# Optimization experiments

Hardware: AMD Instinct MI355X
Metric: run time of the kernel (lower is better)

## Reference

```python
import jax, jax.numpy as jnp
import numpy as np


def setup_inputs() -> dict:
    key = jax.random.key(0)
    k1, k2, k3 = jax.random.split(key, 3)
    B, C, H, W = 16, 256, 32, 32
    K, D = 8192, 256
    z = jax.random.normal(k1, (B, C, H, W), dtype=jnp.float32)
    # torch init: uniform(-1/K, 1/K); use small-scale values for realism
    embedding = jax.random.uniform(k2, (K, D), dtype=jnp.float32,
                                   minval=-1.0 / K, maxval=1.0 / K)
    proj_w = jax.random.normal(k3, (D, D), dtype=jnp.float32) * (1.0 / np.sqrt(D))
    return {"z": z, "embedding": embedding, "proj_w": proj_w}


def reference(z, embedding, proj_w):
    commitment_cost = 0.25
    B, C, H, W = z.shape
    # codebook = Linear(embedding) with no bias: emb @ W^T  -> [K, D]
    codebook = embedding @ proj_w.T
    zt = jnp.transpose(z, (0, 2, 3, 1))            # [B, H, W, C]
    zf = zt.reshape(-1, C)                          # [N, C], N = B*H*W
    # squared distances: ||z||^2 + ||e||^2 - 2 z.e  -> [N, K]
    d = (jnp.sum(zf * zf, axis=1, keepdims=True)
         + jnp.sum(codebook * codebook, axis=1)
         - 2.0 * jnp.einsum('nd,kd->nk', zf, codebook))
    min_encoding_indices = jnp.argmin(d, axis=1)    # [N]
    z_quantized = codebook[min_encoding_indices].reshape(zt.shape)  # [B,H,W,C]
    commitment_loss = commitment_cost * jnp.mean(
        (jax.lax.stop_gradient(z_quantized) - zt) ** 2)
    codebook_loss = jnp.mean((z_quantized - jax.lax.stop_gradient(zt)) ** 2)
    loss = commitment_loss + codebook_loss
    # straight-through estimator
    zq_st = zt + jax.lax.stop_gradient(z_quantized - zt)
    out = jnp.transpose(zq_st, (0, 3, 1, 2))        # [B, C, H, W]
    idx = min_encoding_indices.reshape(B, H, W)
    return out, loss, commitment_loss, codebook_loss, idx
```

## Files before the change

### kernel.cpp

```cpp
#include <hip/hip_runtime.h>
#include <cfloat>


constexpr int Dd = 256;
constexpr float INV_M = 1.0f / 4194304.0f;
constexpr float DLT = 1e-3f;

typedef unsigned short u16;
typedef unsigned int u32;
typedef __attribute__((ext_vector_type(8))) short short8;
typedef __attribute__((ext_vector_type(4))) float f32x4;

#define GLOBAL_AS __attribute__((address_space(1)))
#define LDS_AS    __attribute__((address_space(3)))

__device__ __forceinline__ unsigned monof(float f) {
  unsigned u = __float_as_uint(f);
  return (u & 0x80000000u) ? ~u : (u | 0x80000000u);
}
__device__ __forceinline__ float unmonof(unsigned p) {
  unsigned u = (p & 0x80000000u) ? (p & 0x7FFFFFFFu) : ~p;
  return __uint_as_float(u);
}
__device__ __forceinline__ u16 f2bf(float x) {
  unsigned u = __float_as_uint(x);
  u += 0x7FFFu + ((u >> 16) & 1u);
  return (u16)(u >> 16);
}

__global__ __launch_bounds__(256)
void k_codebook(const float* __restrict__ emb, const float* __restrict__ proj,
                float* __restrict__ cb, u16* __restrict__ eh) {
  __shared__ float et[64 * 65];
  __shared__ float pt[64 * 65];
  const int t = threadIdx.x;
  const int tx = t & 15, ty = t >> 4;
  const int kb = blockIdx.x * 64;
  const int db = blockIdx.y * 64;
  float acc[4][4];
#pragma unroll
  for (int u = 0; u < 4; ++u)
#pragma unroll
    for (int v = 0; v < 4; ++v) acc[u][v] = 0.f;

  const int jm = t & 15;
  const int q  = t >> 4;

  for (int jc = 0; jc < Dd; jc += 64) {
    __syncthreads();
#pragma unroll
    for (int i = 0; i < 4; ++i) {
      const int row = q + i * 16;
      const float4 e4 = *(const float4*)(emb  + (size_t)(kb + row) * Dd + jc + jm * 4);
      const float4 p4 = *(const float4*)(proj + (size_t)(db + row) * Dd + jc + jm * 4);
      et[(jm*4 + 0) * 65 + row] = e4.x;
      et[(jm*4 + 1) * 65 + row] = e4.y;
      et[(jm*4 + 2) * 65 + row] = e4.z;
      et[(jm*4 + 3) * 65 + row] = e4.w;
      pt[(jm*4 + 0) * 65 + row] = p4.x;
      pt[(jm*4 + 1) * 65 + row] = p4.y;
      pt[(jm*4 + 2) * 65 + row] = p4.z;
      pt[(jm*4 + 3) * 65 + row] = p4.w;
    }
    __syncthreads();
#pragma unroll 16
    for (int j = 0; j < 64; ++j) {
      float a[4], b[4];
#pragma unroll
      for (int u = 0; u < 4; ++u) a[u] = et[j*65 + ty*4 + u];
#pragma unroll
      for (int v = 0; v < 4; ++v) b[v] = pt[j*65 + tx*4 + v];
#pragma unroll
      for (int u = 0; u < 4; ++u)
#pragma unroll
        for (int v = 0; v < 4; ++v) acc[u][v] = fmaf(a[u], b[v], acc[u][v]);
    }
  }
#pragma unroll
  for (int u = 0; u < 4; ++u) {
    const int k = kb + ty*4 + u;
#pragma unroll
    for (int v = 0; v < 4; ++v) {
      const int d = db + tx*4 + v;
      const float val = acc[u][v];
      cb[(size_t)k * Dd + d] = val;
      eh[(size_t)k * Dd + d] = f2bf(val);
    }
  }
}

__global__ __launch_bounds__(256)
void k_norms(const float* __restrict__ cb, float* __restrict__ norms) {
  const int k = blockIdx.x * 256 + threadIdx.x;
  const float* row = cb + (size_t)k * Dd;
  float s = 0.f;
  for (int d = 0; d < Dd; d += 4) {
    const float4 v = *(const float4*)(row + d);
    s = fmaf(v.x, v.x, s);
    s = fmaf(v.y, v.y, s);
    s = fmaf(v.z, v.z, s);
    s = fmaf(v.w, v.w, s);
  }
  norms[k] = s;
}

__global__ __launch_bounds__(256)
void k_prep_z(const float* __restrict__ z, u16* __restrict__ zh,
              float* __restrict__ znorm) {
  __shared__ float tile[256 * 33];
  const int t = threadIdx.x;
  const int blk = blockIdx.x;
  const int w = t & 31, rg = t >> 5;
  const size_t zbase = (size_t)(blk >> 5) * 262144 + (size_t)(blk & 31) * 32 + w;
#pragma unroll 8
  for (int i = 0; i < 32; ++i) {
    const int d = rg * 32 + i;
    tile[d * 33 + w] = z[zbase + (size_t)d * 1024];
  }
  __syncthreads();
  if (t < 32) {
    float s = 0.f;
    for (int d = 0; d < Dd; ++d) {
      const float v = tile[d * 33 + t];
      s = fmaf(v, v, s);
    }
    znorm[blk * 32 + t] = s;
  }
  const int nl = t >> 3, seg = t & 7;
  const size_t obase = (size_t)(blk * 32 + nl) * Dd + seg * 32;
#pragma unroll
  for (int j = 0; j < 4; ++j) {
    u16 hb[8];
#pragma unroll
    for (int e = 0; e < 8; ++e)
      hb[e] = f2bf(tile[(seg * 32 + j * 8 + e) * 33 + nl]);
    *(uint4*)(zh + obase + j * 8) = *(const uint4*)hb;
  }
}

template <bool EMIT>
__global__ __launch_bounds__(256, 2)
void k_scan(const u16* __restrict__ zh, const u16* __restrict__ eh,
            const float* __restrict__ norms, const float* __restrict__ znorm,
            u32* __restrict__ rowminG, const float* __restrict__ rowThr,
            u32* __restrict__ rowcnt, u16* __restrict__ slots) {
  __shared__ u16 zs[64 * 256];
  __shared__ u16 es[256 * 64];
  const int t    = threadIdx.x;
  const int lane = t & 63;
  const int ml   = lane & 15;
  const int qd   = lane >> 4;
  const int wvu  = __builtin_amdgcn_readfirstlane(t >> 6);
  const int rowhalf = wvu & 1;
  const int colhalf = wvu >> 1;
  const int bid  = blockIdx.x;
  const int kb   = (bid & 7) * 1024;
  const int nb   = (bid >> 3) * 64;

#pragma unroll
  for (int i = 0; i < 8; ++i) {
    const int r0 = wvu * 16 + i * 2;
    const int row_l = r0 + (lane >> 5);
    const int c = (lane & 31) ^ ((row_l & 7) << 2);
    const u16* gp = zh + (size_t)(nb + row_l) * 256 + c * 8;
    __builtin_amdgcn_global_load_lds((const GLOBAL_AS void*)gp,
                                     (LDS_AS void*)(zs + r0 * 256), 16, 0, 0);
  }

  float zn[2][4], thr[2][4];
#pragma unroll
  for (int rt = 0; rt < 2; ++rt) {
    const int nr = nb + rowhalf * 32 + rt * 16 + qd * 4;
    const f32x4 z4 = *(const f32x4*)(znorm + nr);
#pragma unroll
    for (int r = 0; r < 4; ++r) zn[rt][r] = z4[r];
    if (EMIT) {
      const f32x4 t4 = *(const f32x4*)(rowThr + nr);
#pragma unroll
      for (int r = 0; r < 4; ++r) thr[rt][r] = t4[r];
    }
  }

  float mv[2][4];
#pragma unroll
  for (int rt = 0; rt < 2; ++rt)
#pragma unroll
    for (int r = 0; r < 4; ++r) mv[rt][r] = FLT_MAX;

#pragma unroll 1
  for (int kt = 0; kt < 4; ++kt) {
    f32x4 acc[2][8];
#pragma unroll
    for (int rt = 0; rt < 2; ++rt)
#pragma unroll
      for (int ct = 0; ct < 8; ++ct) acc[rt][ct] = (f32x4)0.f;

#pragma unroll 1
    for (int dh = 0; dh < 4; ++dh) {
      __syncthreads();
#pragma unroll
      for (int i = 0; i < 8; ++i) {
        const int colbase = wvu * 64 + i * 8;
        const int col_l = colbase + (lane >> 3);
        const int c = (lane & 7) ^ (col_l & 7);
        const u16* gp = eh + (size_t)(kb + kt * 256 + col_l) * 256 + dh * 64 + c * 8;
        __builtin_amdgcn_global_load_lds((const GLOBAL_AS void*)gp,
                                         (LDS_AS void*)(es + colbase * 64), 16, 0, 0);
      }
      __syncthreads();

#pragma unroll
      for (int dc2 = 0; dc2 < 2; ++dc2) {
        short8 Af[2], Bf[8];
#pragma unroll
        for (int rt = 0; rt < 2; ++rt) {
          const int row_l = rowhalf * 32 + rt * 16 + ml;
          const int cg = dh * 8 + dc2 * 4 + qd;
          const int slot = cg ^ ((row_l & 7) << 2);
          Af[rt] = *(const short8*)(zs + row_l * 256 + slot * 8);
        }
#pragma unroll
        for (int ct = 0; ct < 8; ++ct) {
          const int col_l = colhalf * 128 + ct * 16 + ml;
          const int c = dc2 * 4 + qd;
          const int slot = c ^ (col_l & 7);
          Bf[ct] = *(const short8*)(es + col_l * 64 + slot * 8);
        }
#pragma unroll
        for (int rt = 0; rt < 2; ++rt)
#pragma unroll
          for (int ct = 0; ct < 8; ++ct)
            acc[rt][ct] = __builtin_amdgcn_mfma_f32_16x16x32_bf16(
                Af[rt], Bf[ct], acc[rt][ct], 0, 0, 0);
      }
    }

#pragma unroll
    for (int ct = 0; ct < 8; ++ct) {
      const int k = kb + kt * 256 + colhalf * 128 + ct * 16 + ml;
      const float nk = norms[k];
#pragma unroll
      for (int rt = 0; rt < 2; ++rt)
#pragma unroll
        for (int r = 0; r < 4; ++r) {
          const float sc = (zn[rt][r] + nk) - 2.0f * acc[rt][ct][r];
          if (!EMIT) {
            mv[rt][r] = fminf(mv[rt][r], sc);
          } else if (sc <= thr[rt][r]) {
            const int n = nb + rowhalf * 32 + rt * 16 + qd * 4 + r;
            const u32 pos = atomicAdd(&rowcnt[n], 1u);
            if (pos < 32u) slots[n * 32 + pos] = (u16)k;
          }
        }
    }
  }

  if (!EMIT) {
#pragma unroll
    for (int rt = 0; rt < 2; ++rt)
#pragma unroll
      for (int r = 0; r < 4; ++r) {
        float m = mv[rt][r];
#pragma unroll
        for (int s = 1; s < 16; s <<= 1) m = fminf(m, __shfl_xor(m, s, 64));
        if (ml == 0)
          atomicMin(&rowminG[nb + rowhalf * 32 + rt * 16 + qd * 4 + r], monof(m));
      }
  }
}

__global__ __launch_bounds__(256)
void k_thresh(const u32* __restrict__ rowminG, float* __restrict__ rowThr) {
  const int n = blockIdx.x * 256 + threadIdx.x;
  rowThr[n] = unmonof(rowminG[n]) + DLT;
}

__global__ __launch_bounds__(256)
void k_rescore(const float* __restrict__ z, const float* __restrict__ cb,
               const float* __restrict__ norms, const float* __restrict__ znorm,
               const u32* __restrict__ rowcnt, const u16* __restrict__ slots,
               unsigned long long* __restrict__ packed) {
  __shared__ float ztl[32 * 261];
  const int t = threadIdx.x;
  const int blk = blockIdx.x;
  const int w = t & 31, dg = t >> 5;
  const size_t zbase = (size_t)(blk >> 5) * 262144 + (size_t)(blk & 31) * 32;
#pragma unroll 8
  for (int i = 0; i < 32; ++i) {
    const int d = dg * 32 + i;
    ztl[w * 261 + d] = z[zbase + (size_t)d * 1024 + w];
  }
  __syncthreads();

  const int lane = t & 63;
  const int wv = t >> 6;
#pragma unroll 1
  for (int i = 0; i < 8; ++i) {
    const int rl = wv * 8 + i;
    const int n = blk * 32 + rl;
    const u32 cnt = min(rowcnt[n], 32u);
    const float znr = znorm[n];
    unsigned long long best = 0xFFFFFFFFFFFFFFFFull;
    for (u32 c = 0; c < cnt; ++c) {
      const int k = (int)slots[n * 32 + c];
      const float4 c4 = *(const float4*)(cb + (size_t)k * Dd + lane * 4);
      const float* zp = ztl + rl * 261 + lane * 4;
      float p = 0.f;
      p = fmaf(zp[0], c4.x, p);
      p = fmaf(zp[1], c4.y, p);
      p = fmaf(zp[2], c4.z, p);
      p = fmaf(zp[3], c4.w, p);
#pragma unroll
      for (int s = 1; s < 64; s <<= 1) p += __shfl_xor(p, s, 64);
      const float sc = (znr + norms[k]) - 2.0f * p;
      const unsigned long long pk =
          ((unsigned long long)monof(sc) << 32) | (unsigned)k;
      if (pk < best) best = pk;
    }
    if (lane == 0 && cnt > 0) packed[n] = best;
  }
}

__global__ __launch_bounds__(256)
void k_output(const float* __restrict__ z, const float* __restrict__ cb,
              const unsigned long long* __restrict__ packed,
              float* __restrict__ out, float* __restrict__ idxf,
              float* __restrict__ ssum) {
  __shared__ float zqT[256 * 33];
  __shared__ float part[4];
  const int t = threadIdx.x;
  const int blk = blockIdx.x;
  const int nbase = blk * 32;

  {
    const int nl = t >> 3, m = t & 7;
    const int idx = (int)(packed[nbase + nl] & 0xFFFFFFFFull);
    const float* row = cb + (size_t)idx * Dd;
#pragma unroll
    for (int i = 0; i < 8; ++i) {
      const int d0 = m * 4 + i * 32;
      const float4 v = *(const float4*)(row + d0);
      zqT[(d0 + 0) * 33 + nl] = v.x;
      zqT[(d0 + 1) * 33 + nl] = v.y;
      zqT[(d0 + 2) * 33 + nl] = v.z;
      zqT[(d0 + 3) * 33 + nl] = v.w;
    }
    if (t < 32)
      idxf[nbase + t] = (float)(unsigned)(packed[nbase + t] & 0xFFFFFFFFull);
  }
  __syncthreads();

  const int w = t & 31, cg = t >> 5;
  const size_t base = (size_t)(blk >> 5) * 262144 + (size_t)(blk & 31) * 32 + w;
  float local = 0.f;
#pragma unroll
  for (int cc = 0; cc < 32; ++cc) {
    const int c = cg * 32 + cc;
    const float q  = zqT[c * 33 + w];
    const float zv = z[base + (size_t)c * 1024];
    out[base + (size_t)c * 1024] = q;
    const float dd = q - zv;
    local = fmaf(dd, dd, local);
  }
  float v = local;
#pragma unroll
  for (int m = 1; m < 64; m <<= 1) v += __shfl_xor(v, m, 64);
  if ((t & 63) == 0) part[t >> 6] = v;
  __syncthreads();
  if (t == 0) atomicAdd(ssum, part[0] + part[1] + part[2] + part[3]);
}

__global__ void k_final(const float* __restrict__ ssum, float* __restrict__ scal) {
  const float m = *ssum * INV_M;
  scal[0] = 1.25f * m;
  scal[1] = 0.25f * m;
  scal[2] = m;
}

extern "C" void kernel_launch(void* const* d_in, const int* in_sizes, int n_in,
                              void* d_out, int out_size, void* d_ws, size_t ws_size,
                              hipStream_t stream) {
  const float* z    = (const float*)d_in[0];
  const float* emb  = (const float*)d_in[1];
  const float* proj = (const float*)d_in[2];

  float* out  = (float*)d_out;
  float* scal = out + 4194304;
  float* idxf = out + 4194307;

  float* cb    = (float*)d_ws;
  float* norms = cb + 2097152;
  unsigned long long* packed =
      (unsigned long long*)(norms + 8192);
  float* znorm = (float*)(packed + 16384);
  u16* zh = (u16*)(znorm + 16384);
  u16* eh = zh + 4194304;
  u32* rowminG = (u32*)(eh + 2097152);
  float* rowThr = (float*)(rowminG + 16384);
  u32* rowcnt = (u32*)(rowThr + 16384);
  u16* slots = (u16*)(rowcnt + 16384);
  float* ssum = (float*)(slots + 16384 * 32);

  hipMemsetAsync(rowminG, 0xFF, 16384 * sizeof(u32), stream);
  hipMemsetAsync(rowcnt, 0, 16384 * sizeof(u32), stream);
  hipMemsetAsync(packed, 0xFF, 16384 * sizeof(unsigned long long), stream);
  hipMemsetAsync(ssum, 0, sizeof(float), stream);

  k_codebook<<<dim3(128, 4), 256, 0, stream>>>(emb, proj, cb, eh);
  k_norms   <<<32, 256, 0, stream>>>(cb, norms);
  k_prep_z  <<<512, 256, 0, stream>>>(z, zh, znorm);
  k_scan<false><<<2048, 256, 0, stream>>>(zh, eh, norms, znorm,
                                          rowminG, rowThr, rowcnt, slots);
  k_thresh  <<<64, 256, 0, stream>>>(rowminG, rowThr);
  k_scan<true> <<<2048, 256, 0, stream>>>(zh, eh, norms, znorm,
                                          rowminG, rowThr, rowcnt, slots);
  k_rescore <<<512, 256, 0, stream>>>(z, cb, norms, znorm, rowcnt, slots, packed);
  k_output  <<<512, 256, 0, stream>>>(z, cb, packed, out, idxf, ssum);
  k_final   <<<1, 1, 0, stream>>>(ssum, scal);

  (void)in_sizes; (void)n_in; (void)out_size; (void)ws_size;
}
```

Measured before the change: 401.2 us.

## Double-buffer codebook LDS tiles and prefetch next chunk during MFMA

The codebook staging buffer is split into two half-size buffers, each holding a 32-element slice of the feature dimension. The next slice is loaded asynchronously into one buffer while MFMAs consume the other, and the inner loop is fully unrolled. This hides global-to-LDS load latency and cuts barriers from two per step to one. The LDS layout now packs pairs of codebook rows with a new XOR swizzle. It relies on the barrier waiting for outstanding LDS-DMA loads, and each step now has a smaller compute chunk.

```diff
diff --git a/kernel.cpp b/kernel.cpp
--- a/kernel.cpp
+++ b/kernel.cpp
@@ -144,8 +144,8 @@
             const float* __restrict__ norms, const float* __restrict__ znorm,
             u32* __restrict__ rowminG, const float* __restrict__ rowThr,
             u32* __restrict__ rowcnt, u16* __restrict__ slots) {
-  __shared__ u16 zs[64 * 256];
-  __shared__ u16 es[256 * 64];
+  __shared__ __align__(16) u16 zs[64 * 256];
+  __shared__ __align__(16) u16 es[2][256 * 32];
   const int t    = threadIdx.x;
   const int lane = t & 63;
   const int ml   = lane & 15;
@@ -167,6 +167,25 @@
                                      (LDS_AS void*)(zs + r0 * 256), 16, 0, 0);
   }
 
+  const u16* gb[4];
+  int eld[4];
+#pragma unroll
+  for (int i = 0; i < 4; ++i) {
+    const int cp  = wvu * 32 + i * 8 + (lane >> 3);
+    const int v   = (lane & 7) ^ (cp & 7);
+    const int col = cp * 2 + (v >> 2);
+    gb[i]  = eh + (size_t)(kb + col) * 256 + (v & 3) * 8;
+    eld[i] = (wvu * 32 + i * 8) * 64;
+  }
+  auto stage_es = [&](int buf, int ktv, int dhv) {
+    const int goff = ktv * 65536 + dhv * 32;
+#pragma unroll
+    for (int i = 0; i < 4; ++i)
+      __builtin_amdgcn_global_load_lds((const GLOBAL_AS void*)(gb[i] + goff),
+                                       (LDS_AS void*)(&es[buf][eld[i]]), 16, 0, 0);
+  };
+  stage_es(0, 0, 0);
+
   float zn[2][4], thr[2][4];
 #pragma unroll
   for (int rt = 0; rt < 2; ++rt) {
@@ -195,44 +214,34 @@
 #pragma unroll
       for (int ct = 0; ct < 8; ++ct) acc[rt][ct] = (f32x4)0.f;
 
-#pragma unroll 1
-    for (int dh = 0; dh < 4; ++dh) {
+#pragma unroll
+    for (int dhp = 0; dhp < 8; ++dhp) {
       __syncthreads();
-#pragma unroll
-      for (int i = 0; i < 8; ++i) {
-        const int colbase = wvu * 64 + i * 8;
-        const int col_l = colbase + (lane >> 3);
-        const int c = (lane & 7) ^ (col_l & 7);
-        const u16* gp = eh + (size_t)(kb + kt * 256 + col_l) * 256 + dh * 64 + c * 8;
-        __builtin_amdgcn_global_load_lds((const GLOBAL_AS void*)gp,
-                                         (LDS_AS void*)(es + colbase * 64), 16, 0, 0);
+      const int tn = kt * 8 + dhp + 1;
+      if (tn < 32) stage_es((dhp + 1) & 1, tn >> 3, tn & 7);
+
+      const u16* eb = es[dhp & 1];
+      short8 Af[2], Bf[8];
+#pragma unroll
+      for (int rt = 0; rt < 2; ++rt) {
+        const int row_l = rowhalf * 32 + rt * 16 + ml;
+        const int cg = dhp * 4 + qd;
+        const int slot = cg ^ ((row_l & 7) << 2);
+        Af[rt] = *(const short8*)(zs + row_l * 256 + slot * 8);
       }
-      __syncthreads();
-
-#pragma unroll
-      for (int dc2 = 0; dc2 < 2; ++dc2) {
-        short8 Af[2], Bf[8];
-#pragma unroll
-        for (int rt = 0; rt < 2; ++rt) {
-          const int row_l = rowhalf * 32 + rt * 16 + ml;
-          const int cg = dh * 8 + dc2 * 4 + qd;
-          const int slot = cg ^ ((row_l & 7) << 2);
-          Af[rt] = *(const short8*)(zs + row_l * 256 + slot * 8);
-        }
-#pragma unroll
-        for (int ct = 0; ct < 8; ++ct) {
-          const int col_l = colhalf * 128 + ct * 16 + ml;
-          const int c = dc2 * 4 + qd;
-          const int slot = c ^ (col_l & 7);
-          Bf[ct] = *(const short8*)(es + col_l * 64 + slot * 8);
-        }
-#pragma unroll
-        for (int rt = 0; rt < 2; ++rt)
-#pragma unroll
-          for (int ct = 0; ct < 8; ++ct)
-            acc[rt][ct] = __builtin_amdgcn_mfma_f32_16x16x32_bf16(
-                Af[rt], Bf[ct], acc[rt][ct], 0, 0, 0);
+#pragma unroll
+      for (int ct = 0; ct < 8; ++ct) {
+        const int col_l = colhalf * 128 + ct * 16 + ml;
+        const int cp = col_l >> 1;
+        const int sl = ((col_l & 1) * 4 + qd) ^ (cp & 7);
+        Bf[ct] = *(const short8*)(eb + cp * 64 + sl * 8);
       }
+#pragma unroll
+      for (int rt = 0; rt < 2; ++rt)
+#pragma unroll
+        for (int ct = 0; ct < 8; ++ct)
+          acc[rt][ct] = __builtin_amdgcn_mfma_f32_16x16x32_bf16(
+              Af[rt], Bf[ct], acc[rt][ct], 0, 0, 0);
     }
 
 #pragma unroll
```

New measurement: 412.7 us. +2.9%, slower.

## Load codebook MFMA fragments directly from global into registers with double buffering

Applied to the files above, without the earlier changes.

Drops the LDS staging of the codebook tile and its per-chunk barriers. Each lane now loads its B fragments straight from global memory into registers, ping-ponging between two register sets to prefetch the next 32-wide depth chunk while the current one feeds the MFMAs. Codebook norms are also loaded at the top of each column tile. This removes LDS traffic and synchronisation, but it raises register pressure, adds global/L2 load latency per fragment, and loses cross-wave reuse of the codebook tile inside the block.

```diff
diff --git a/kernel.cpp b/kernel.cpp
--- a/kernel.cpp
+++ b/kernel.cpp
@@ -144,8 +144,7 @@
             const float* __restrict__ norms, const float* __restrict__ znorm,
             u32* __restrict__ rowminG, const float* __restrict__ rowThr,
             u32* __restrict__ rowcnt, u16* __restrict__ slots) {
-  __shared__ u16 zs[64 * 256];
-  __shared__ u16 es[256 * 64];
+  __shared__ __align__(16) u16 zs[64 * 256];
   const int t    = threadIdx.x;
   const int lane = t & 63;
   const int ml   = lane & 15;
@@ -166,6 +165,9 @@
     __builtin_amdgcn_global_load_lds((const GLOBAL_AS void*)gp,
                                      (LDS_AS void*)(zs + r0 * 256), 16, 0, 0);
   }
+  __syncthreads();
+
+  const u16* eb = eh + (size_t)(kb + colhalf * 128 + ml) * 256 + qd * 8;
 
   float zn[2][4], thr[2][4];
 #pragma unroll
@@ -187,63 +189,75 @@
 #pragma unroll
     for (int r = 0; r < 4; ++r) mv[rt][r] = FLT_MAX;
 
+  short8 B0[8], B1[8];
+#pragma unroll
+  for (int ct = 0; ct < 8; ++ct)
+    B0[ct] = *(const short8*)(eb + ct * 4096);
+
 #pragma unroll 1
   for (int kt = 0; kt < 4; ++kt) {
+    float nk[8];
+#pragma unroll
+    for (int ct = 0; ct < 8; ++ct)
+      nk[ct] = norms[kb + kt * 256 + colhalf * 128 + ct * 16 + ml];
+
     f32x4 acc[2][8];
 #pragma unroll
     for (int rt = 0; rt < 2; ++rt)
 #pragma unroll
       for (int ct = 0; ct < 8; ++ct) acc[rt][ct] = (f32x4)0.f;
 
-#pragma unroll 1
-    for (int dh = 0; dh < 4; ++dh) {
-      __syncthreads();
-#pragma unroll
-      for (int i = 0; i < 8; ++i) {
-        const int colbase = wvu * 64 + i * 8;
-        const int col_l = colbase + (lane >> 3);
-        const int c = (lane & 7) ^ (col_l & 7);
-        const u16* gp = eh + (size_t)(kb + kt * 256 + col_l) * 256 + dh * 64 + c * 8;
-        __builtin_amdgcn_global_load_lds((const GLOBAL_AS void*)gp,
-                                         (LDS_AS void*)(es + colbase * 64), 16, 0, 0);
+#pragma unroll
+    for (int dhp = 0; dhp < 8; ++dhp) {
+      if (kt * 8 + dhp + 1 < 32) {
+        const int pn = kt * 8 + dhp + 1;
+        const int offn = (pn >> 3) * 65536 + (pn & 7) * 32;
+        if (dhp & 1) {
+#pragma unroll
+          for (int ct = 0; ct < 8; ++ct)
+            B0[ct] = *(const short8*)(eb + ct * 4096 + offn);
+        } else {
+#pragma unroll
+          for (int ct = 0; ct < 8; ++ct)
+            B1[ct] = *(const short8*)(eb + ct * 4096 + offn);
+        }
       }
-      __syncthreads();
-
-#pragma unroll
-      for (int dc2 = 0; dc2 < 2; ++dc2) {
-        short8 Af[2], Bf[8];
-#pragma unroll
-        for (int rt = 0; rt < 2; ++rt) {
-          const int row_l = rowhalf * 32 + rt * 16 + ml;
-          const int cg = dh * 8 + dc2 * 4 + qd;
-          const int slot = cg ^ ((row_l & 7) << 2);
-          Af[rt] = *(const short8*)(zs + row_l * 256 + slot * 8);
-        }
-#pragma unroll
-        for (int ct = 0; ct < 8; ++ct) {
-          const int col_l = colhalf * 128 + ct * 16 + ml;
-          const int c = dc2 * 4 + qd;
-          const int slot = c ^ (col_l & 7);
-          Bf[ct] = *(const short8*)(es + col_l * 64 + slot * 8);
-        }
+
+      short8 Af[2];
+#pragma unroll
+      for (int rt = 0; rt < 2; ++rt) {
+        const int row_l = rowhalf * 32 + rt * 16 + ml;
+        const int cg = dhp * 4 + qd;
+        const int slot = cg ^ ((row_l & 7) << 2);
+        Af[rt] = *(const short8*)(zs + row_l * 256 + slot * 8);
+      }
+
+      if (dhp & 1) {
 #pragma unroll
         for (int rt = 0; rt < 2; ++rt)
 #pragma unroll
           for (int ct = 0; ct < 8; ++ct)
             acc[rt][ct] = __builtin_amdgcn_mfma_f32_16x16x32_bf16(
-                Af[rt], Bf[ct], acc[rt][ct], 0, 0, 0);
+                Af[rt], B1[ct], acc[rt][ct], 0, 0, 0);
+      } else {
+#pragma unroll
+        for (int rt = 0; rt < 2; ++rt)
+#pragma unroll
+          for (int ct = 0; ct < 8; ++ct)
+            acc[rt][ct] = __builtin_amdgcn_mfma_f32_16x16x32_bf16(
+                Af[rt], B0[ct], acc[rt][ct], 0, 0, 0);
       }
     }
 
 #pragma unroll
     for (int ct = 0; ct < 8; ++ct) {
       const int k = kb + kt * 256 + colhalf * 128 + ct * 16 + ml;
-      const float nk = norms[k];
+      const float nkv = nk[ct];
 #pragma unroll
       for (int rt = 0; rt < 2; ++rt)
 #pragma unroll
         for (int r = 0; r < 4; ++r) {
-          const float sc = (zn[rt][r] + nk) - 2.0f * acc[rt][ct][r];
+          const float sc = (zn[rt][r] + nkv) - 2.0f * acc[rt][ct][r];
           if (!EMIT) {
             mv[rt][r] = fminf(mv[rt][r], sc);
           } else if (sc <= thr[rt][r]) {
```

Result: slower. 675.0 us (+68.2%).
